# Kernel optimization log

Hardware: AMD Instinct MI355X
Metric: run time of the kernel (lower is better)

## Reference

```python
import jax, jax.numpy as jnp
import numpy as np
from jax import lax

# program token ids
PAD, START, END, SCENE, INTERSECT, FILT, RELATE, QUERY = range(8)
SKIP = (PAD, START, END)


def conv2d(x, w, b, dil=1):
    # 'same' padding for odd kernels (3x3 pad=dil, 1x1 pad=0), NCHW/OIHW
    pad = dil * (w.shape[2] // 2)
    y = lax.conv_general_dilated(x, w, (1, 1), [(pad, pad), (pad, pad)],
                                 rhs_dilation=(dil, dil),
                                 dimension_numbers=('NCHW', 'OIHW', 'NCHW'))
    return y + b[None, :, None, None]


def maxpool2(x):
    return lax.reduce_window(x, -jnp.inf, lax.max, (1, 1, 2, 2), (1, 1, 2, 2), 'VALID')


def exec_program(prog, feat_input, p):
    """Run one (concrete) program over a batch of stem features. prog: tuple of ints,
    executed in reversed order exactly like TbDNet.forward."""
    B, _, H, W = feat_input.shape
    output = feat_input
    saved = None
    for t in reversed(prog):
        if t in SKIP:
            continue
        if t == SCENE:
            saved = output
            output = jnp.ones((B, 1, H, W), feat_input.dtype)
        elif t == INTERSECT:  # AndModule: elementwise min of attentions
            output = jnp.minimum(output, saved)
        elif t == FILT:
            a = feat_input * output  # [B,D,H,W] * [B,1,H,W]
            a = jax.nn.relu(conv2d(a, p['att_w1'], p['att_b1']))
            a = jax.nn.relu(conv2d(a, p['att_w2'], p['att_b2']))
            output = jax.nn.sigmoid(conv2d(a, p['att_w3'], p['att_b3']))
        elif t == RELATE:  # RelateModule: dilated conv stack (1,2,4,8,1) -> conv1x1 sigmoid
            a = feat_input * output
            for w, b, d in ((p['rel_w1'], p['rel_b1'], 1), (p['rel_w2'], p['rel_b2'], 2),
                            (p['rel_w3'], p['rel_b3'], 4), (p['rel_w4'], p['rel_b4'], 8),
                            (p['rel_w5'], p['rel_b5'], 1)):
                a = jax.nn.relu(conv2d(a, w, b, d))
            output = jax.nn.sigmoid(conv2d(a, p['rel_w6'], p['rel_b6']))
        elif t == QUERY:
            a = feat_input * output
            a = jax.nn.relu(conv2d(a, p['qry_w1'], p['qry_b1']))
            output = jax.nn.relu(conv2d(a, p['qry_w2'], p['qry_b2']))
    return output


def tbd_forward(feats, programs_np, p):
    B = feats.shape[0]
    stem = jax.nn.relu(conv2d(feats, p['stem_w1'], p['stem_b1']))
    stem = jax.nn.relu(conv2d(stem, p['stem_w2'], p['stem_b2']))  # [B,D,H,W]
    D, H, W = stem.shape[1], stem.shape[2], stem.shape[3]
    # group samples by identical program so dispatch runs batched, not per-sample
    groups = {}
    for n in range(B):
        groups.setdefault(tuple(int(v) for v in programs_np[n]), []).append(n)
    mod_out = jnp.zeros((B, D, H, W), feats.dtype)
    for prog, idxs in groups.items():
        idx = jnp.array(idxs)
        mod_out = mod_out.at[idx].set(exec_program(prog, stem[idx], p))
    # classifier: conv1x1 -> relu -> maxpool2 -> flatten -> fc -> relu -> fc
    x = jax.nn.relu(conv2d(mod_out, p['cls_w'], p['cls_b']))
    x = maxpool2(x)                        # [B,1024,7,7]
    x = x.reshape(B, -1)                   # [B,50176]
    x = jax.nn.relu(x @ p['fc1_w'].T + p['fc1_b'])
    return x @ p['fc2_w'].T + p['fc2_b']   # [B,28]


def setup_inputs() -> dict:
    key = jax.random.key(0)
    ks = iter(jax.random.split(key, 64))
    def rn(shape, s=0.05):
        return jax.random.normal(next(ks), shape, dtype=jnp.float32) * s
    B, Cin, H, W, D, P, L, A = 64, 1024, 14, 14, 128, 1024, 1024, 28
    feats = jax.random.normal(next(ks), (B, Cin, H, W), dtype=jnp.float32)
    # stored programs; execution order is reversed(stored)
    progA = [START, QUERY, FILT, RELATE, FILT, SCENE, END, PAD]            # scene->filter->relate->filter->query
    progB = [START, QUERY, INTERSECT, FILT, SCENE, FILT, SCENE, END]       # two filter branches -> intersect -> query
    programs = jnp.array([progA] * (B // 2) + [progB] * (B // 2), dtype=jnp.int32)
    inp = {'feats': feats, 'programs': programs,
           'stem_w1': rn((D, Cin, 3, 3), 0.02), 'stem_b1': rn((D,)),
           'stem_w2': rn((D, D, 3, 3)), 'stem_b2': rn((D,)),
           'att_w1': rn((D, D, 3, 3)), 'att_b1': rn((D,)),
           'att_w2': rn((D, D, 3, 3)), 'att_b2': rn((D,)),
           'att_w3': rn((1, D, 1, 1)), 'att_b3': rn((1,)),
           'rel_w1': rn((D, D, 3, 3)), 'rel_b1': rn((D,)),
           'rel_w2': rn((D, D, 3, 3)), 'rel_b2': rn((D,)),
           'rel_w3': rn((D, D, 3, 3)), 'rel_b3': rn((D,)),
           'rel_w4': rn((D, D, 3, 3)), 'rel_b4': rn((D,)),
           'rel_w5': rn((D, D, 3, 3)), 'rel_b5': rn((D,)),
           'rel_w6': rn((1, D, 1, 1)), 'rel_b6': rn((1,)),
           'qry_w1': rn((D, D, 3, 3)), 'qry_b1': rn((D,)),
           'qry_w2': rn((D, D, 3, 3)), 'qry_b2': rn((D,)),
           'cls_w': rn((P, D, 1, 1)), 'cls_b': rn((P,)),
           'fc1_w': rn((L, P * (H // 2) * (W // 2)), 0.01), 'fc1_b': rn((L,)),
           'fc2_w': rn((A, L)), 'fc2_b': rn((A,))}
    return inp


PARAM_NAMES = ['stem_w1', 'stem_b1', 'stem_w2', 'stem_b2',
               'att_w1', 'att_b1', 'att_w2', 'att_b2', 'att_w3', 'att_b3',
               'rel_w1', 'rel_b1', 'rel_w2', 'rel_b2', 'rel_w3', 'rel_b3',
               'rel_w4', 'rel_b4', 'rel_w5', 'rel_b5', 'rel_w6', 'rel_b6',
               'qry_w1', 'qry_b1', 'qry_w2', 'qry_b2',
               'cls_w', 'cls_b', 'fc1_w', 'fc1_b', 'fc2_w', 'fc2_b']


def reference(feats, programs, stem_w1, stem_b1, stem_w2, stem_b2,
              att_w1, att_b1, att_w2, att_b2, att_w3, att_b3,
              rel_w1, rel_b1, rel_w2, rel_b2, rel_w3, rel_b3,
              rel_w4, rel_b4, rel_w5, rel_b5, rel_w6, rel_b6,
              qry_w1, qry_b1, qry_w2, qry_b2,
              cls_w, cls_b, fc1_w, fc1_b, fc2_w, fc2_b):
    vals = [stem_w1, stem_b1, stem_w2, stem_b2,
            att_w1, att_b1, att_w2, att_b2, att_w3, att_b3,
            rel_w1, rel_b1, rel_w2, rel_b2, rel_w3, rel_b3,
            rel_w4, rel_b4, rel_w5, rel_b5, rel_w6, rel_b6,
            qry_w1, qry_b1, qry_w2, qry_b2,
            cls_w, cls_b, fc1_w, fc1_b, fc2_w, fc2_b]
    p = dict(zip(PARAM_NAMES, vals))
    return tbd_forward(feats, np.asarray(programs), p)
```

## Files before the change

### kernel.cpp

```cpp
#include <hip/hip_runtime.h>
#include <math.h>


typedef __attribute__((ext_vector_type(8)))  short   short8;
typedef __attribute__((ext_vector_type(8)))  __bf16  bf16x8;
typedef __attribute__((ext_vector_type(4)))  float   f32x4;

#define NROUNDS 11
#define NKS 98
#define S1KS 16

#define B_WSTEM1 0UL
#define B_WSTEM2 2359296UL
#define B_WMOD   2654208UL
#define B_WCLS   5308416UL
#define B_STEM   5570560UL
#define B_XA     8781824UL
#define B_XB     11993088UL
#define B_FEAT   15204352UL
#define B_ATTN   18415616UL
#define B_SAVED  18465792UL
#define B_SCHED  18515968UL
#define B_ACTB   18520064UL
#define B_FC1T   24942592UL
#define B_P1X1   25204736UL
#define B_S1P    67108864UL
#define B_FC1P   134217728UL

__device__ __forceinline__ unsigned short f2bf(float f) {
    __bf16 h = (__bf16)f;
    union { __bf16 h; unsigned short u; } c; c.h = h; return c.u;
}
__device__ __forceinline__ float bf2f(unsigned short u) {
    return __uint_as_float(((unsigned int)u) << 16);
}
__device__ __forceinline__ unsigned int pkbf(float a, float b) {
    return (unsigned int)f2bf(a) | ((unsigned int)f2bf(b) << 16);
}
__device__ __forceinline__ f32x4 mfma16(bf16x8 a, bf16x8 b, f32x4 c) {
    return __builtin_amdgcn_mfma_f32_16x16x32_bf16(a, b, c, 0, 0, 0);
}

struct PrepArgs { const float* src[12]; const int* prog; char* ws; };

__global__ __launch_bounds__(256) void k_prep(PrepArgs a)
{
    char* ws = a.ws;
    const int bx = blockIdx.x;
    if (bx < 768) {
        const int y = bx >> 6;
        const float* __restrict__ src = a.src[y];
        int gid = (bx & 63) * 256 + threadIdx.x;
        int gsz = 64 * 256;
        if (y == 11) {
            unsigned short* dst = (unsigned short*)(ws + B_WCLS);
            for (int i = gid; i < 131072; i += gsz) dst[i] = f2bf(src[i]);
        } else {
            const int IC = (y == 0) ? 1024 : 128;
            const int lg = (y == 0) ? 10 : 7;
            unsigned short* dst = (unsigned short*)(ws + ((y == 0) ? B_WSTEM1
                                        : (y == 1) ? B_WSTEM2
                                        : B_WMOD + (size_t)(y - 2) * 294912));
            const int total = 9 << (lg + 7);
            for (int i = gid; i < total; i += gsz) {
                int ic = i & (IC - 1);
                int oc = (i >> lg) & 127;
                int t  = i >> (lg + 7);
                dst[i] = f2bf(src[((size_t)oc * IC + ic) * 9 + t]);
            }
        }
        return;
    }
    int gid = (bx - 768) * 256 + threadIdx.x;
    int gsz = 256 * 256;
    float* attn  = (float*)(ws + B_ATTN);
    float* saved = (float*)(ws + B_SAVED);
    float* p1    = (float*)(ws + B_P1X1);
    for (int i = gid; i < 64 * 196; i += gsz) { attn[i] = 1.0f; saved[i] = 1.0f; }
    for (int i = gid; i < 8 * 64 * 196; i += gsz) p1[i] = 0.0f;
    unsigned int* fz = (unsigned int*)(ws + B_FEAT);
    for (int i = gid; i < 64 * 25088 / 2; i += gsz) fz[i] = 0u;
    if (gid < 64) {
        int n = gid;
        const int* prog = a.prog;
        int ent[NROUNDS];
        for (int r = 0; r < NROUNDS; ++r) ent[r] = 0;
        int rc = 0, nslot = 0;
        int pscene = 0, pinter = 0, pmat = 0, pmw = 0;
#define PREBITS ((pscene<<17)|(pinter<<18)|(pmat<<19)|(pmw<<22))
#define CLRPRE  (pscene = pinter = pmat = pmw = 0)
#define EMIT(v) do { if (rc < NROUNDS) ent[rc++] = (v); } while (0)
        for (int j = 7; j >= 0; --j) {
            int t = prog[n * 8 + j];
            switch (t) {
                case 3: pscene = 1; break;
                case 4: pinter = 1; break;
                case 5: {
                    int e1 = 3 | (0<<4) | (1<<8) | (1<<12) | (2<<13) | (0<<15) | PREBITS;
                    CLRPRE; EMIT(e1);
                    EMIT(3 | (1<<4) | (1<<8) | (0<<12) | (0<<13) | (1<<15)
                           | (1<<23) | (0<<24) | (nslot<<25));
                    pmat = nslot + 1; pmw = 0; nslot++;
                    break;
                }
                case 6: {
                    int e1 = 3 | (2<<4) | (1<<8) | (1<<12) | (2<<13) | (0<<15) | PREBITS;
                    CLRPRE; EMIT(e1);
                    EMIT(3 | (3<<4) | (2<<8) | (0<<12) | (0<<13) | (1<<15));
                    EMIT(3 | (4<<4) | (4<<8) | (0<<12) | (1<<13) | (0<<15));
                    EMIT(3 | (5<<4) | (8<<8) | (0<<12) | (0<<13) | (1<<15));
                    EMIT(3 | (6<<4) | (1<<8) | (0<<12) | (1<<13) | (0<<15)
                           | (1<<23) | (1<<24) | (nslot<<25));
                    pmat = nslot + 1; pmw = 1; nslot++;
                    break;
                }
                case 7: {
                    int e1 = 3 | (7<<4) | (1<<8) | (1<<12) | (2<<13) | (0<<15) | PREBITS;
                    CLRPRE; EMIT(e1);
                    EMIT(3 | (8<<4) | (1<<8) | (0<<12) | (0<<13) | (2<<15));
                    break;
                }
                default: break;
            }
        }
#undef EMIT
#undef PREBITS
#undef CLRPRE
        int* sched = (int*)(ws + B_SCHED);
        for (int r = 0; r < NROUNDS; ++r) sched[n * NROUNDS + r] = ent[r];
    }
}

__global__ __launch_bounds__(512) void k_stem1p(const float* __restrict__ feats,
                                                const unsigned short* __restrict__ wrep,
                                                char* ws)
{
    __shared__ unsigned short s_img[197 * 72];
    const int bx = blockIdx.x;
    const int n = bx >> 4, ks = bx & 15;
    const int tid = threadIdx.x, lane = tid & 63;
    const int w = tid >> 6, wm = w & 1, wn = w >> 1;
    const int l15 = lane & 15, lq = lane >> 4;

    if (tid < 36) ((unsigned int*)(s_img + 196 * 72))[tid] = 0u;

    int pglob[4], pbyt[4], pyv[4], pxv[4];
#pragma unroll
    for (int j = 0; j < 4; ++j) {
        int p  = (wn + 4 * j) * 16 + l15;
        pglob[j] = p;
        int py = p / 14;
        pyv[j] = (p < 196) ? py : 10000;
        pxv[j] = p - py * 14;
        pbyt[j] = p * 144 + lq * 16;
    }
    const int zaddr = 196 * 144 + lq * 16;
    const int nJ = (wn == 0) ? 4 : 3;

    f32x4 acc[4][4];
#pragma unroll
    for (int m = 0; m < 4; ++m)
#pragma unroll
        for (int j = 0; j < 4; ++j) acc[m][j] = (f32x4){0.f, 0.f, 0.f, 0.f};

    const int icg = tid & 15;
    const int qq0 = tid >> 4;
    const int icb = ks * 64;

    const float* sf = feats + ((size_t)n * 1024 + icb) * 196;
    for (int qq = qq0; qq < 49; qq += 32) {
        const float* p0 = sf + icg * 4 * 196 + qq * 4;
        float4 r0 = *(const float4*)(p0);
        float4 r1 = *(const float4*)(p0 + 196);
        float4 r2 = *(const float4*)(p0 + 392);
        float4 r3 = *(const float4*)(p0 + 588);
#pragma unroll
        for (int e = 0; e < 4; ++e) {
            uint2 v;
            v.x = pkbf(((const float*)&r0)[e], ((const float*)&r1)[e]);
            v.y = pkbf(((const float*)&r2)[e], ((const float*)&r3)[e]);
            *(uint2*)(s_img + (qq * 4 + e) * 72 + icg * 4) = v;
        }
    }
    __syncthreads();

#pragma unroll
    for (int t = 0; t < 9; ++t) {
        const int dy = t / 3 - 1, dx = t % 3 - 1;
        int baddr[4];
#pragma unroll
        for (int j = 0; j < 4; ++j) {
            int yy = pyv[j] + dy, xx = pxv[j] + dx;
            bool ok = ((unsigned)yy < 14u) && ((unsigned)xx < 14u);
            baddr[j] = ok ? (pbyt[j] + (dy * 14 + dx) * 144) : zaddr;
        }
#pragma unroll
        for (int kc = 0; kc < 2; ++kc) {
            const unsigned short* wt = wrep +
                ((size_t)(t * 128 + wm * 64 + l15) * 1024 + icb + kc * 32 + lq * 8);
            bf16x8 am[4];
#pragma unroll
            for (int m = 0; m < 4; ++m)
                am[m] = *(const bf16x8*)(wt + (size_t)m * 16 * 1024);
#pragma unroll
            for (int j = 0; j < 4; ++j) {
                if (j < nJ) {
                    bf16x8 b = *(const bf16x8*)((const char*)s_img + baddr[j] + kc * 64);
#pragma unroll
                    for (int m = 0; m < 4; ++m)
                        acc[m][j] = mfma16(am[m], b, acc[m][j]);
                }
            }
        }
    }

    unsigned short* part = (unsigned short*)(ws + B_S1P);
#pragma unroll
    for (int m = 0; m < 4; ++m) {
        const int oc = wm * 64 + m * 16 + lq * 4;
#pragma unroll
        for (int j = 0; j < 4; ++j) {
            if (j < nJ) {
                int p = pglob[j];
                if (p < 196) {
                    uint2 pk;
                    pk.x = pkbf(acc[m][j][0], acc[m][j][1]);
                    pk.y = pkbf(acc[m][j][2], acc[m][j][3]);
                    *(uint2*)(part + (((size_t)ks * 64 + n) * 196 + p) * 128 + oc) = pk;
                }
            }
        }
    }
}

__global__ __launch_bounds__(256) void k_stem1r(const char* __restrict__ ws_c,
                                                const float* __restrict__ bias,
                                                unsigned short* __restrict__ xa)
{
    int i = blockIdx.x * 256 + threadIdx.x;
    const unsigned short* part = (const unsigned short*)(ws_c + B_S1P);
    int oc8 = (i & 15) * 8;
    int np  = i >> 4;
    float s[8] = {};
#pragma unroll
    for (int ks = 0; ks < S1KS; ++ks) {
        short8 v = *(const short8*)(part + (((size_t)ks * 64) * 196 + np) * 128 + oc8);
#pragma unroll
        for (int e = 0; e < 8; ++e) s[e] += bf2f((unsigned short)v[e]);
    }
    short8 o;
#pragma unroll
    for (int e = 0; e < 8; ++e)
        o[e] = (short)f2bf(fmaxf(s[e] + bias[oc8 + e], 0.f));
    *(short8*)(xa + (size_t)np * 128 + oc8) = o;
}

__device__ void conv_core32(const unsigned short* __restrict__ srcB,
                            const float* __restrict__ s_gate,
                            const unsigned short* __restrict__ wrep,
                            const float* __restrict__ bias,
                            unsigned short* __restrict__ dst,
                            int dil, int oct, int pxh,
                            unsigned short* s_img,
                            int post, const float* __restrict__ pwv,
                            float* __restrict__ pdst)
{
    const int tid  = threadIdx.x, lane = tid & 63;
    const int w    = tid >> 6, wm = w & 1, wn = w >> 1;
    const int l15  = lane & 15, lq = lane >> 4;

    if (tid < 68) ((unsigned int*)s_img)[196 * 68 + tid] = 0u;

    int pglob[4], pbyt[4], pyv[4], pxv[4];
#pragma unroll
    for (int j = 0; j < 4; ++j) {
        int nt = wn + 2 * j;
        int p  = (pxh * 7 + nt) * 16 + l15;
        pglob[j] = p;
        int py = p / 14;
        pyv[j] = (p < 196) ? py : 10000;
        pxv[j] = p - py * 14;
        pbyt[j] = p * 272 + lq * 16;
    }
    const int zaddr = 196 * 272 + lq * 16;
    const int nNT = (wn == 0) ? 4 : 3;

    f32x4 acc[4];
#pragma unroll
    for (int j = 0; j < 4; ++j) acc[j] = (f32x4){0.f, 0.f, 0.f, 0.f};

    if (s_gate) {
        for (int i = tid; i < 196 * 16; i += 256) {
            int p = i >> 4, c8 = (i & 15) * 8;
            short8 v = *(const short8*)(srcB + p * 128 + c8);
            float g = s_gate[p];
            uint2 o0, o1;
            o0.x = pkbf(bf2f((unsigned short)v[0]) * g, bf2f((unsigned short)v[1]) * g);
            o0.y = pkbf(bf2f((unsigned short)v[2]) * g, bf2f((unsigned short)v[3]) * g);
            o1.x = pkbf(bf2f((unsigned short)v[4]) * g, bf2f((unsigned short)v[5]) * g);
            o1.y = pkbf(bf2f((unsigned short)v[6]) * g, bf2f((unsigned short)v[7]) * g);
            *(uint2*)(s_img + p * 136 + c8)     = o0;
            *(uint2*)(s_img + p * 136 + c8 + 4) = o1;
        }
    } else {
        for (int i = tid; i < 196 * 16; i += 256) {
            int p = i >> 4, c8 = (i & 15) * 8;
            *(short8*)(s_img + p * 136 + c8) = *(const short8*)(srcB + p * 128 + c8);
        }
    }
    __syncthreads();

    const unsigned short* wlane = wrep + (size_t)(oct * 32 + wm * 16 + l15) * 128 + lq * 8;
#pragma unroll
    for (int t = 0; t < 9; ++t) {
        const int dy = (t / 3 - 1) * dil, dx = (t % 3 - 1) * dil;
        int baddr[4];
#pragma unroll
        for (int j = 0; j < 4; ++j) {
            int yy = pyv[j] + dy, xx = pxv[j] + dx;
            bool ok = ((unsigned)yy < 14u) && ((unsigned)xx < 14u);
            baddr[j] = ok ? (pbyt[j] + (dy * 14 + dx) * 272) : zaddr;
        }
        const unsigned short* wt = wlane + (size_t)(t * 128) * 128;
#pragma unroll
        for (int kc = 0; kc < 4; ++kc) {
            bf16x8 a0 = *(const bf16x8*)(wt + kc * 32);
#pragma unroll
            for (int j = 0; j < 4; ++j) {
                if (j < nNT) {
                    bf16x8 b = *(const bf16x8*)((const char*)s_img + baddr[j] + kc * 64);
                    acc[j] = mfma16(a0, b, acc[j]);
                }
            }
        }
    }

    const int oc = oct * 32 + wm * 16 + lq * 4;
    const float4 b4 = *(const float4*)(bias + oc);
    float4 wv4;
    if (post) wv4 = *(const float4*)(pwv + oc);
#pragma unroll
    for (int j = 0; j < 4; ++j) {
        if (j < nNT) {
            int p = pglob[j];
            if (p < 196) {
                float v0 = fmaxf(acc[j][0] + b4.x, 0.f);
                float v1 = fmaxf(acc[j][1] + b4.y, 0.f);
                float v2 = fmaxf(acc[j][2] + b4.z, 0.f);
                float v3 = fmaxf(acc[j][3] + b4.w, 0.f);
                uint2 pk;
                pk.x = pkbf(v0, v1);
                pk.y = pkbf(v2, v3);
                *(uint2*)(dst + p * 128 + oc) = pk;
                if (post) {
                    float s = v0 * wv4.x + v1 * wv4.y + v2 * wv4.z + v3 * wv4.w;
                    atomicAdd(pdst + p, s);
                }
            }
        }
    }
}

__global__ __launch_bounds__(256) void k_conv_stem2(const unsigned short* __restrict__ srcBall,
                                                    const unsigned short* __restrict__ wrep,
                                                    const float* __restrict__ bias,
                                                    unsigned short* __restrict__ dstall)
{
    __shared__ unsigned short s_img[197 * 136];
    const int n = blockIdx.x >> 3, oct = (blockIdx.x >> 1) & 3, pxh = blockIdx.x & 1;
    conv_core32(srcBall + (size_t)n * 25088, nullptr, wrep, bias,
                dstall + (size_t)n * 25088, 1, oct, pxh, s_img, 0, nullptr, nullptr);
}

struct RArgs {
    char* ws;
    const float* mbias[9];
    const float* w1x1[2];
    const float* b1x1[2];
};

__global__ __launch_bounds__(256) void k_round(RArgs a, int r)
{
    __shared__ unsigned short s_img[197 * 136];
    __shared__ float s_gate[196];
    const int bx = blockIdx.x;
    const int n = bx >> 3, oct = (bx >> 1) & 3, pxh = bx & 1;
    char* ws = a.ws;
    const int* sched = (const int*)(ws + B_SCHED);
    const int e = sched[n * NROUNDS + r];
    if ((e & 15) == 0) return;
    const int tid = threadIdx.x;
    const int wset = (e >> 4) & 15, dil = (e >> 8) & 15, gatef = (e >> 12) & 1;
    const int srcid = (e >> 13) & 3, dstid = (e >> 15) & 3;
    const int fscene = (e >> 17) & 1, finter = (e >> 18) & 1;
    const int mslot = (e >> 19) & 7, mw = (e >> 22) & 1;
    const int post = (e >> 23) & 1, pw = (e >> 24) & 1, pslot = (e >> 25) & 7;

    float* attn  = (float*)(ws + B_ATTN)  + n * 196;
    float* saved = (float*)(ws + B_SAVED) + n * 196;
    float* p1    = (float*)(ws + B_P1X1);

    if (gatef) {
        if (tid < 196) {
            float cur = attn[tid];
            if (mslot) {
                float pv = p1[(size_t)(mslot - 1) * 12544 + n * 196 + tid];
                cur = 1.0f / (1.0f + __expf(-(pv + a.b1x1[mw][0])));
            }
            if (fscene) { saved[tid] = cur; cur = 1.0f; }
            if (finter) { cur = fminf(cur, saved[tid]); }
            if (mslot | fscene | finter) attn[tid] = cur;
            s_gate[tid] = cur;
        }
        __syncthreads();
    }

    const unsigned short* src = (const unsigned short*)(ws +
            (srcid == 2 ? B_STEM : srcid == 1 ? B_XB : B_XA)) + (size_t)n * 25088;
    unsigned short* dst = (unsigned short*)(ws +
            (dstid == 2 ? B_FEAT : dstid == 1 ? B_XB : B_XA)) + (size_t)n * 25088;
    const unsigned short* wrep = (const unsigned short*)(ws + B_WMOD) + (size_t)wset * 9 * 128 * 128;

    conv_core32(src, gatef ? s_gate : nullptr, wrep, a.mbias[wset], dst,
                dil, oct, pxh, s_img,
                post, post ? a.w1x1[pw] : nullptr,
                post ? (p1 + (size_t)pslot * 12544 + n * 196) : nullptr);
}

__global__ __launch_bounds__(256) void k_cls_pool(const unsigned short* __restrict__ featall,
                                                  const unsigned short* __restrict__ clsw,
                                                  const float* __restrict__ clsb,
                                                  unsigned short* __restrict__ actB)
{
    __shared__ char smem[197 * 272 + 64 * 200 * 4];
    unsigned short* s_img = (unsigned short*)smem;
    float* s_pool = (float*)(smem + 197 * 272);
    const int n = blockIdx.x >> 4, pt = blockIdx.x & 15;
    const int tid = threadIdx.x, lane = tid & 63, w = tid >> 6;
    const int l15 = lane & 15, lq = lane >> 4;
    const unsigned short* feat = featall + (size_t)n * 25088;

    if (tid < 68) ((unsigned int*)s_img)[196 * 68 + tid] = 0u;
    for (int i = tid; i < 196 * 16; i += 256) {
        int p = i >> 4, c8 = (i & 15) * 8;
        *(short8*)(s_img + p * 136 + c8) = *(const short8*)(feat + p * 128 + c8);
    }
    f32x4 acc[14];
#pragma unroll
    for (int j = 0; j < 14; ++j) acc[j] = (f32x4){0.f, 0.f, 0.f, 0.f};
    __syncthreads();

    const unsigned short* wl = clsw + (size_t)(pt * 64 + w * 16 + l15) * 128 + lq * 8;
#pragma unroll
    for (int kc = 0; kc < 4; ++kc) {
        bf16x8 a0 = *(const bf16x8*)(wl + kc * 32);
#pragma unroll
        for (int j = 0; j < 14; ++j) {
            int p = j * 16 + l15;
            int ba = (p < 196) ? (p * 272 + lq * 16 + kc * 64) : (196 * 272 + lq * 16);
            bf16x8 b = *(const bf16x8*)((const char*)s_img + ba);
            acc[j] = mfma16(a0, b, acc[j]);
        }
    }
    const int oc = pt * 64 + w * 16 + lq * 4;
    const float4 b4 = *(const float4*)(clsb + oc);
    const int pl = w * 16 + lq * 4;
#pragma unroll
    for (int j = 0; j < 14; ++j) {
        int p = j * 16 + l15;
        if (p < 196) {
            s_pool[(pl + 0) * 200 + p] = fmaxf(acc[j][0] + b4.x, 0.f);
            s_pool[(pl + 1) * 200 + p] = fmaxf(acc[j][1] + b4.y, 0.f);
            s_pool[(pl + 2) * 200 + p] = fmaxf(acc[j][2] + b4.z, 0.f);
            s_pool[(pl + 3) * 200 + p] = fmaxf(acc[j][3] + b4.w, 0.f);
        }
    }
    __syncthreads();
    for (int i = tid; i < 64 * 49; i += 256) {
        int plx = i / 49, q = i - plx * 49;
        int py = q / 7, qx = q - py * 7;
        const float* rp = s_pool + plx * 200 + py * 28 + qx * 2;
        float m = fmaxf(fmaxf(rp[0], rp[1]), fmaxf(rp[14], rp[15]));
        int k = (pt * 64 + plx) * 49 + q;
        int kb = k >> 6, lq2 = (k >> 4) & 3, hi = (k >> 3) & 1, e = k & 7;
        actB[((((size_t)kb * 4 + lq2) * 2 + hi) * 64 + n) * 8 + e] = f2bf(m);
    }
}

__global__ __launch_bounds__(256) void k_fc1p(const unsigned short* __restrict__ actB,
                                              const float* __restrict__ w,
                                              float* __restrict__ part)
{
    __shared__ unsigned short s_w[64 * 264];
    const int jt = blockIdx.x & 15, ks = blockIdx.x >> 4;
    const int tid = threadIdx.x, lane = tid & 63, wv = tid >> 6;
    const int l15 = lane & 15, lq = lane >> 4;
    const int k0 = ks * 512;

    f32x4 acc[4];
#pragma unroll
    for (int t = 0; t < 4; ++t) acc[t] = (f32x4){0.f, 0.f, 0.f, 0.f};

    float4 pf[16];

#define FC1_LOAD(ss_) do {                                                        \
    _Pragma("unroll")                                                             \
    for (int pass = 0; pass < 16; ++pass) {                                       \
        const int row_ = pass * 4 + wv;                                           \
        pf[pass] = *(const float4*)(w + (size_t)(jt * 64 + row_) * 50176 + k0     \
                                      + (ss_) * 256 + lane * 4);                  \
    } } while (0)

    FC1_LOAD(0);

    for (int ss = 0; ss < 2; ++ss) {
        __syncthreads();
#pragma unroll
        for (int pass = 0; pass < 16; ++pass) {
            const int row = pass * 4 + wv;
            uint2 v;
            v.x = pkbf(pf[pass].x, pf[pass].y);
            v.y = pkbf(pf[pass].z, pf[pass].w);
            *(uint2*)(s_w + row * 264 + lane * 4) = v;
        }
        __syncthreads();
        if (ss < 1) FC1_LOAD(1);

        const unsigned short* arow = s_w + (wv * 16 + l15) * 264;
#pragma unroll
        for (int kk = 0; kk < 8; ++kk) {
            bf16x8 a = *(const bf16x8*)(arow + kk * 32 + lq * 8);
            const int kglob = k0 + ss * 256 + kk * 32 + lq * 8;
            const int kb = kglob >> 6, lq2 = (kglob >> 4) & 3, hi = (kglob >> 3) & 1;
            const unsigned short* bp = actB +
                ((((size_t)kb * 4 + lq2) * 2 + hi) * 64 + l15) * 8;
#pragma unroll
            for (int t = 0; t < 4; ++t) {
                bf16x8 b = *(const bf16x8*)(bp + t * 128);
                acc[t] = mfma16(a, b, acc[t]);
            }
        }
    }
#undef FC1_LOAD

    float* pbase = part + ((size_t)ks * 1024 + jt * 64 + wv * 16 + lq * 4) * 64 + l15;
#pragma unroll
    for (int t = 0; t < 4; ++t)
#pragma unroll
        for (int r = 0; r < 4; ++r)
            pbase[(size_t)r * 64 + t * 16] = acc[t][r];
}

__global__ __launch_bounds__(256) void k_fc1r(const float* __restrict__ part,
                                              const float* __restrict__ b,
                                              float* __restrict__ fc1T)
{
    int i = blockIdx.x * 256 + threadIdx.x;
    if (i >= 65536) return;
    float s = 0.0f;
    for (int ks = 0; ks < NKS; ++ks) s += part[(size_t)ks * 65536 + i];
    int j = i >> 6;
    fc1T[i] = fmaxf(s + b[j], 0.0f);
}

__global__ __launch_bounds__(256) void k_fc2(const float* __restrict__ fc1T,
                                             const float* __restrict__ w,
                                             const float* __restrict__ b,
                                             float* __restrict__ out)
{
    __shared__ float red[256];
    const int a_ = blockIdx.x;
    const int tid = threadIdx.x, lane = tid & 63, q = tid >> 6;
    float acc = 0.0f;
    const float* wr = w + (size_t)a_ * 1024;
    for (int k = q * 256; k < q * 256 + 256; ++k)
        acc = fmaf(fc1T[k * 64 + lane], wr[k], acc);
    red[tid] = acc;
    __syncthreads();
    if (q == 0) {
        float s = red[tid] + red[tid + 64] + red[tid + 128] + red[tid + 192] + b[a_];
        out[lane * 28 + a_] = s;
    }
}

extern "C" void kernel_launch(void* const* d_in, const int* in_sizes, int n_in,
                              void* d_out, int out_size, void* d_ws, size_t ws_size,
                              hipStream_t stream)
{
    const float* feats = (const float*)d_in[0];
    const int*   prog  = (const int*)d_in[1];
    char* ws  = (char*)d_ws;
    float* out = (float*)d_out;

    PrepArgs pa;
    pa.src[0]  = (const float*)d_in[2];
    pa.src[1]  = (const float*)d_in[4];
    pa.src[2]  = (const float*)d_in[6];
    pa.src[3]  = (const float*)d_in[8];
    pa.src[4]  = (const float*)d_in[12];
    pa.src[5]  = (const float*)d_in[14];
    pa.src[6]  = (const float*)d_in[16];
    pa.src[7]  = (const float*)d_in[18];
    pa.src[8]  = (const float*)d_in[20];
    pa.src[9]  = (const float*)d_in[24];
    pa.src[10] = (const float*)d_in[26];
    pa.src[11] = (const float*)d_in[28];
    pa.prog = prog;
    pa.ws = ws;
    k_prep<<<1024, 256, 0, stream>>>(pa);

    k_stem1p<<<1024, 512, 0, stream>>>(feats, (const unsigned short*)(ws + B_WSTEM1), ws);
    k_stem1r<<<784, 256, 0, stream>>>(ws, (const float*)d_in[3],
                                      (unsigned short*)(ws + B_XA));

    k_conv_stem2<<<512, 256, 0, stream>>>((const unsigned short*)(ws + B_XA),
                                          (const unsigned short*)(ws + B_WSTEM2),
                                          (const float*)d_in[5],
                                          (unsigned short*)(ws + B_STEM));

    RArgs ga;
    ga.ws = ws;
    ga.mbias[0] = (const float*)d_in[7];
    ga.mbias[1] = (const float*)d_in[9];
    ga.mbias[2] = (const float*)d_in[13];
    ga.mbias[3] = (const float*)d_in[15];
    ga.mbias[4] = (const float*)d_in[17];
    ga.mbias[5] = (const float*)d_in[19];
    ga.mbias[6] = (const float*)d_in[21];
    ga.mbias[7] = (const float*)d_in[25];
    ga.mbias[8] = (const float*)d_in[27];
    ga.w1x1[0]  = (const float*)d_in[10];
    ga.w1x1[1]  = (const float*)d_in[22];
    ga.b1x1[0]  = (const float*)d_in[11];
    ga.b1x1[1]  = (const float*)d_in[23];

    for (int r = 0; r < NROUNDS; ++r)
        k_round<<<512, 256, 0, stream>>>(ga, r);

    k_cls_pool<<<1024, 256, 0, stream>>>((const unsigned short*)(ws + B_FEAT),
                                         (const unsigned short*)(ws + B_WCLS),
                                         (const float*)d_in[29],
                                         (unsigned short*)(ws + B_ACTB));
    k_fc1p<<<1568, 256, 0, stream>>>((const unsigned short*)(ws + B_ACTB),
                                     (const float*)d_in[30], (float*)(ws + B_FC1P));
    k_fc1r<<<256, 256, 0, stream>>>((const float*)(ws + B_FC1P), (const float*)d_in[31],
                                    (float*)(ws + B_FC1T));
    k_fc2<<<28, 256, 0, stream>>>((const float*)(ws + B_FC1T), (const float*)d_in[32],
                                  (const float*)d_in[33], out);
}
```

Measured before the change: 514.7 us.

## Fuse paired 3x3 convs of Filter/Query modules into one round via shared-memory intermediate

Adds a fused op (op 5) that runs the first conv of the attention and query modules over all 128 output channels into shared memory, then runs the second conv from that buffer. This cuts the schedule from 11 to 8 rounds and avoids a global round-trip for the intermediate activation. Each block now handles a whole image with 512 threads, with 256 blocks instead of 512. In exchange the first conv is recomputed redundantly in each of the 4 output-channel blocks, and fewer blocks run per launch.

```diff
diff --git a/kernel.cpp b/kernel.cpp
--- a/kernel.cpp
+++ b/kernel.cpp
@@ -6,7 +6,7 @@
 typedef __attribute__((ext_vector_type(8)))  __bf16  bf16x8;
 typedef __attribute__((ext_vector_type(4)))  float   f32x4;
 
-#define NROUNDS 11
+#define NROUNDS 8
 #define NKS 98
 #define S1KS 16
 
@@ -96,28 +96,26 @@
                 case 3: pscene = 1; break;
                 case 4: pinter = 1; break;
                 case 5: {
-                    int e1 = 3 | (0<<4) | (1<<8) | (1<<12) | (2<<13) | (0<<15) | PREBITS;
+                    int e1 = 5 | (0<<4) | (1<<8) | (1<<12) | (0<<15) | PREBITS
+                               | (1<<23) | (0<<24) | (nslot<<25);
                     CLRPRE; EMIT(e1);
-                    EMIT(3 | (1<<4) | (1<<8) | (0<<12) | (0<<13) | (1<<15)
-                           | (1<<23) | (0<<24) | (nslot<<25));
                     pmat = nslot + 1; pmw = 0; nslot++;
                     break;
                 }
                 case 6: {
                     int e1 = 3 | (2<<4) | (1<<8) | (1<<12) | (2<<13) | (0<<15) | PREBITS;
                     CLRPRE; EMIT(e1);
-                    EMIT(3 | (3<<4) | (2<<8) | (0<<12) | (0<<13) | (1<<15));
-                    EMIT(3 | (4<<4) | (4<<8) | (0<<12) | (1<<13) | (0<<15));
-                    EMIT(3 | (5<<4) | (8<<8) | (0<<12) | (0<<13) | (1<<15));
-                    EMIT(3 | (6<<4) | (1<<8) | (0<<12) | (1<<13) | (0<<15)
+                    EMIT(3 | (3<<4) | (2<<8) | (0<<13) | (1<<15));
+                    EMIT(3 | (4<<4) | (4<<8) | (1<<13) | (0<<15));
+                    EMIT(3 | (5<<4) | (8<<8) | (0<<13) | (1<<15));
+                    EMIT(3 | (6<<4) | (1<<8) | (1<<13) | (0<<15)
                            | (1<<23) | (1<<24) | (nslot<<25));
                     pmat = nslot + 1; pmw = 1; nslot++;
                     break;
                 }
                 case 7: {
-                    int e1 = 3 | (7<<4) | (1<<8) | (1<<12) | (2<<13) | (0<<15) | PREBITS;
+                    int e1 = 5 | (7<<4) | (8<<8) | (1<<12) | (2<<15) | PREBITS;
                     CLRPRE; EMIT(e1);
-                    EMIT(3 | (8<<4) | (1<<8) | (0<<12) | (0<<13) | (2<<15));
                     break;
                 }
                 default: break;
@@ -256,14 +254,11 @@
 }
 
 __device__ void conv_core32(const unsigned short* __restrict__ srcB,
-                            const float* __restrict__ s_gate,
                             const unsigned short* __restrict__ wrep,
                             const float* __restrict__ bias,
                             unsigned short* __restrict__ dst,
-                            int dil, int oct, int pxh,
-                            unsigned short* s_img,
-                            int post, const float* __restrict__ pwv,
-                            float* __restrict__ pdst)
+                            int oct, int pxh,
+                            unsigned short* s_img)
 {
     const int tid  = threadIdx.x, lane = tid & 63;
     const int w    = tid >> 6, wm = w & 1, wn = w >> 1;
@@ -289,10 +284,210 @@
 #pragma unroll
     for (int j = 0; j < 4; ++j) acc[j] = (f32x4){0.f, 0.f, 0.f, 0.f};
 
-    if (s_gate) {
-        for (int i = tid; i < 196 * 16; i += 256) {
+    for (int i = tid; i < 196 * 16; i += 256) {
+        int p = i >> 4, c8 = (i & 15) * 8;
+        *(short8*)(s_img + p * 136 + c8) = *(const short8*)(srcB + p * 128 + c8);
+    }
+    __syncthreads();
+
+    const unsigned short* wlane = wrep + (size_t)(oct * 32 + wm * 16 + l15) * 128 + lq * 8;
+#pragma unroll
+    for (int t = 0; t < 9; ++t) {
+        const int dy = t / 3 - 1, dx = t % 3 - 1;
+        int baddr[4];
+#pragma unroll
+        for (int j = 0; j < 4; ++j) {
+            int yy = pyv[j] + dy, xx = pxv[j] + dx;
+            bool ok = ((unsigned)yy < 14u) && ((unsigned)xx < 14u);
+            baddr[j] = ok ? (pbyt[j] + (dy * 14 + dx) * 272) : zaddr;
+        }
+        const unsigned short* wt = wlane + (size_t)(t * 128) * 128;
+#pragma unroll
+        for (int kc = 0; kc < 4; ++kc) {
+            bf16x8 a0 = *(const bf16x8*)(wt + kc * 32);
+#pragma unroll
+            for (int j = 0; j < 4; ++j) {
+                if (j < nNT) {
+                    bf16x8 b = *(const bf16x8*)((const char*)s_img + baddr[j] + kc * 64);
+                    acc[j] = mfma16(a0, b, acc[j]);
+                }
+            }
+        }
+    }
+
+    const int oc = oct * 32 + wm * 16 + lq * 4;
+    const float4 b4 = *(const float4*)(bias + oc);
+#pragma unroll
+    for (int j = 0; j < 4; ++j) {
+        if (j < nNT) {
+            int p = pglob[j];
+            if (p < 196) {
+                uint2 pk;
+                pk.x = pkbf(fmaxf(acc[j][0] + b4.x, 0.f), fmaxf(acc[j][1] + b4.y, 0.f));
+                pk.y = pkbf(fmaxf(acc[j][2] + b4.z, 0.f), fmaxf(acc[j][3] + b4.w, 0.f));
+                *(uint2*)(dst + p * 128 + oc) = pk;
+            }
+        }
+    }
+}
+
+__global__ __launch_bounds__(256) void k_conv_stem2(const unsigned short* __restrict__ srcBall,
+                                                    const unsigned short* __restrict__ wrep,
+                                                    const float* __restrict__ bias,
+                                                    unsigned short* __restrict__ dstall)
+{
+    __shared__ unsigned short s_img[197 * 136];
+    const int n = blockIdx.x >> 3, oct = (blockIdx.x >> 1) & 3, pxh = blockIdx.x & 1;
+    conv_core32(srcBall + (size_t)n * 25088, wrep, bias,
+                dstall + (size_t)n * 25088, oct, pxh, s_img);
+}
+
+struct RArgs {
+    char* ws;
+    const float* mbias[9];
+    const float* w1x1[2];
+    const float* b1x1[2];
+};
+
+__global__ __launch_bounds__(512) void k_round(RArgs a, int r)
+{
+    __shared__ unsigned short s_img[197 * 136];
+    __shared__ unsigned short s_tmp[197 * 136];
+    __shared__ float s_gate[196];
+    const int bx = blockIdx.x;
+    const int n = bx >> 2, oct = bx & 3;
+    char* ws = a.ws;
+    const int* sched = (const int*)(ws + B_SCHED);
+    const int e = sched[n * NROUNDS + r];
+    const int op = e & 15;
+    if (op == 0) return;
+    const int tid = threadIdx.x, lane = tid & 63;
+    const int w = tid >> 6, wm = w & 1, wn = w >> 1;
+    const int l15 = lane & 15, lq = lane >> 4;
+    const int wset1 = (e >> 4) & 15, f8 = (e >> 8) & 15, gatef = (e >> 12) & 1;
+    const int srcid = (e >> 13) & 3, dstid = (e >> 15) & 3;
+    const int fscene = (e >> 17) & 1, finter = (e >> 18) & 1;
+    const int mslot = (e >> 19) & 7, mw = (e >> 22) & 1;
+    const int post = (e >> 23) & 1, pw = (e >> 24) & 1, pslot = (e >> 25) & 7;
+
+    float* attn  = (float*)(ws + B_ATTN)  + n * 196;
+    float* saved = (float*)(ws + B_SAVED) + n * 196;
+    float* p1    = (float*)(ws + B_P1X1);
+
+    if (tid < 68) ((unsigned int*)s_img)[196 * 68 + tid] = 0u;
+    else if (tid < 136) ((unsigned int*)s_tmp)[196 * 68 + (tid - 68)] = 0u;
+
+    if (gatef && tid < 196) {
+        float cur = attn[tid];
+        if (mslot) {
+            float pv = p1[(size_t)(mslot - 1) * 12544 + n * 196 + tid];
+            cur = 1.0f / (1.0f + __expf(-(pv + a.b1x1[mw][0])));
+        }
+        if (fscene) { saved[tid] = cur; cur = 1.0f; }
+        if (finter) { cur = fminf(cur, saved[tid]); }
+        if (mslot | fscene | finter) attn[tid] = cur;
+        s_gate[tid] = cur;
+    }
+    __syncthreads();
+
+    const int zaddr = 196 * 272 + lq * 16;
+    const unsigned short* wmod = (const unsigned short*)(ws + B_WMOD);
+
+    if (op == 3) {
+        const unsigned short* src = (const unsigned short*)(ws +
+                (srcid == 2 ? B_STEM : srcid == 1 ? B_XB : B_XA)) + (size_t)n * 25088;
+        if (gatef) {
+            for (int i = tid; i < 196 * 16; i += 512) {
+                int p = i >> 4, c8 = (i & 15) * 8;
+                short8 v = *(const short8*)(src + p * 128 + c8);
+                float g = s_gate[p];
+                uint2 o0, o1;
+                o0.x = pkbf(bf2f((unsigned short)v[0]) * g, bf2f((unsigned short)v[1]) * g);
+                o0.y = pkbf(bf2f((unsigned short)v[2]) * g, bf2f((unsigned short)v[3]) * g);
+                o1.x = pkbf(bf2f((unsigned short)v[4]) * g, bf2f((unsigned short)v[5]) * g);
+                o1.y = pkbf(bf2f((unsigned short)v[6]) * g, bf2f((unsigned short)v[7]) * g);
+                *(uint2*)(s_img + p * 136 + c8)     = o0;
+                *(uint2*)(s_img + p * 136 + c8 + 4) = o1;
+            }
+        } else {
+            for (int i = tid; i < 196 * 16; i += 512) {
+                int p = i >> 4, c8 = (i & 15) * 8;
+                *(short8*)(s_img + p * 136 + c8) = *(const short8*)(src + p * 128 + c8);
+            }
+        }
+        __syncthreads();
+
+        int pglob[4], pbyt[4], pyv[4], pxv[4];
+#pragma unroll
+        for (int j = 0; j < 4; ++j) {
+            int p = (wn + 4 * j) * 16 + l15;
+            pglob[j] = p;
+            int py = p / 14;
+            pyv[j] = (p < 196) ? py : 10000;
+            pxv[j] = p - py * 14;
+            pbyt[j] = p * 272 + lq * 16;
+        }
+        const int nJ = (wn == 0) ? 4 : 3;
+        f32x4 acc[4];
+#pragma unroll
+        for (int j = 0; j < 4; ++j) acc[j] = (f32x4){0.f, 0.f, 0.f, 0.f};
+
+        const int dil = f8;
+        const unsigned short* wlane = wmod + (size_t)wset1 * 147456 / 2 * 0;
+        wlane = wmod + (size_t)wset1 * 9 * 128 * 128
+                     + (size_t)(oct * 32 + wm * 16 + l15) * 128 + lq * 8;
+#pragma unroll
+        for (int t = 0; t < 9; ++t) {
+            const int dy = (t / 3 - 1) * dil, dx = (t % 3 - 1) * dil;
+            int ba[4];
+#pragma unroll
+            for (int j = 0; j < 4; ++j) {
+                int yy = pyv[j] + dy, xx = pxv[j] + dx;
+                bool ok = ((unsigned)yy < 14u) && ((unsigned)xx < 14u);
+                ba[j] = ok ? (pbyt[j] + (dy * 14 + dx) * 272) : zaddr;
+            }
+            const unsigned short* wt = wlane + (size_t)(t * 128) * 128;
+#pragma unroll
+            for (int kc = 0; kc < 4; ++kc) {
+                bf16x8 a0 = *(const bf16x8*)(wt + kc * 32);
+#pragma unroll
+                for (int j = 0; j < 4; ++j) {
+                    if (j < nJ) {
+                        bf16x8 b = *(const bf16x8*)((const char*)s_img + ba[j] + kc * 64);
+                        acc[j] = mfma16(a0, b, acc[j]);
+                    }
+                }
+            }
+        }
+
+        unsigned short* dst = (unsigned short*)(ws +
+                (dstid == 2 ? B_FEAT : dstid == 1 ? B_XB : B_XA)) + (size_t)n * 25088;
+        const int oc = oct * 32 + wm * 16 + lq * 4;
+        const float4 b4 = *(const float4*)(a.mbias[wset1] + oc);
+        float4 wv4;
+        if (post) wv4 = *(const float4*)(a.w1x1[pw] + oc);
+        float* pdst = p1 + (size_t)pslot * 12544 + n * 196;
+#pragma unroll
+        for (int j = 0; j < 4; ++j) {
+            if (j < nJ) {
+                int p = pglob[j];
+                if (p < 196) {
+                    float v0 = fmaxf(acc[j][0] + b4.x, 0.f);
+                    float v1 = fmaxf(acc[j][1] + b4.y, 0.f);
+                    float v2 = fmaxf(acc[j][2] + b4.z, 0.f);
+                    float v3 = fmaxf(acc[j][3] + b4.w, 0.f);
+                    uint2 pk; pk.x = pkbf(v0, v1); pk.y = pkbf(v2, v3);
+                    *(uint2*)(dst + p * 128 + oc) = pk;
+                    if (post)
+                        atomicAdd(pdst + p, v0 * wv4.x + v1 * wv4.y + v2 * wv4.z + v3 * wv4.w);
+                }
+            }
+        }
+    } else {
+        const unsigned short* stem = (const unsigned short*)(ws + B_STEM) + (size_t)n * 25088;
+        for (int i = tid; i < 196 * 16; i += 512) {
             int p = i >> 4, c8 = (i & 15) * 8;
-            short8 v = *(const short8*)(srcB + p * 128 + c8);
+            short8 v = *(const short8*)(stem + p * 128 + c8);
             float g = s_gate[p];
             uint2 o0, o1;
             o0.x = pkbf(bf2f((unsigned short)v[0]) * g, bf2f((unsigned short)v[1]) * g);
@@ -302,129 +497,125 @@
             *(uint2*)(s_img + p * 136 + c8)     = o0;
             *(uint2*)(s_img + p * 136 + c8 + 4) = o1;
         }
-    } else {
-        for (int i = tid; i < 196 * 16; i += 256) {
-            int p = i >> 4, c8 = (i & 15) * 8;
-            *(short8*)(s_img + p * 136 + c8) = *(const short8*)(srcB + p * 128 + c8);
-        }
-    }
-    __syncthreads();
-
-    const unsigned short* wlane = wrep + (size_t)(oct * 32 + wm * 16 + l15) * 128 + lq * 8;
-#pragma unroll
-    for (int t = 0; t < 9; ++t) {
-        const int dy = (t / 3 - 1) * dil, dx = (t % 3 - 1) * dil;
-        int baddr[4];
+        __syncthreads();
+
+        const unsigned short* w1 = wmod + (size_t)wset1 * 9 * 128 * 128;
+        int pg2[13], pb2[13], pyv2[13], pxv2[13];
+#pragma unroll
+        for (int j2 = 0; j2 < 13; ++j2) {
+            int p = j2 * 16 + l15;
+            pg2[j2] = p;
+            int py = p / 14;
+            pyv2[j2] = (p < 196) ? py : 10000;
+            pxv2[j2] = p - py * 14;
+            pb2[j2] = p * 272 + lq * 16;
+        }
+        f32x4 acc1[13];
+#pragma unroll
+        for (int j2 = 0; j2 < 13; ++j2) acc1[j2] = (f32x4){0.f, 0.f, 0.f, 0.f};
+#pragma unroll
+        for (int t = 0; t < 9; ++t) {
+            const int dy = t / 3 - 1, dx = t % 3 - 1;
+            int ba[13];
+#pragma unroll
+            for (int j2 = 0; j2 < 13; ++j2) {
+                int yy = pyv2[j2] + dy, xx = pxv2[j2] + dx;
+                bool ok = ((unsigned)yy < 14u) && ((unsigned)xx < 14u);
+                ba[j2] = ok ? (pb2[j2] + (dy * 14 + dx) * 272) : zaddr;
+            }
+#pragma unroll
+            for (int kc = 0; kc < 4; ++kc) {
+                bf16x8 av = *(const bf16x8*)(w1 +
+                    (size_t)(t * 128 + w * 16 + l15) * 128 + kc * 32 + lq * 8);
+#pragma unroll
+                for (int j2 = 0; j2 < 13; ++j2) {
+                    bf16x8 b = *(const bf16x8*)((const char*)s_img + ba[j2] + kc * 64);
+                    acc1[j2] = mfma16(av, b, acc1[j2]);
+                }
+            }
+        }
+        {
+            const int oc1 = w * 16 + lq * 4;
+            const float4 b14 = *(const float4*)(a.mbias[wset1] + oc1);
+#pragma unroll
+            for (int j2 = 0; j2 < 13; ++j2) {
+                int p = pg2[j2];
+                if (p < 196) {
+                    uint2 pk;
+                    pk.x = pkbf(fmaxf(acc1[j2][0] + b14.x, 0.f),
+                                fmaxf(acc1[j2][1] + b14.y, 0.f));
+                    pk.y = pkbf(fmaxf(acc1[j2][2] + b14.z, 0.f),
+                                fmaxf(acc1[j2][3] + b14.w, 0.f));
+                    *(uint2*)(s_tmp + p * 136 + oc1) = pk;
+                }
+            }
+        }
+        __syncthreads();
+
+        const unsigned short* w2base = wmod + (size_t)f8 * 9 * 128 * 128
+                     + (size_t)(oct * 32 + wm * 16 + l15) * 128 + lq * 8;
+        int pglob[4], pbyt[4], pyv[4], pxv[4];
 #pragma unroll
         for (int j = 0; j < 4; ++j) {
-            int yy = pyv[j] + dy, xx = pxv[j] + dx;
-            bool ok = ((unsigned)yy < 14u) && ((unsigned)xx < 14u);
-            baddr[j] = ok ? (pbyt[j] + (dy * 14 + dx) * 272) : zaddr;
-        }
-        const unsigned short* wt = wlane + (size_t)(t * 128) * 128;
-#pragma unroll
-        for (int kc = 0; kc < 4; ++kc) {
-            bf16x8 a0 = *(const bf16x8*)(wt + kc * 32);
+            int p = (wn + 4 * j) * 16 + l15;
+            pglob[j] = p;
+            int py = p / 14;
+            pyv[j] = (p < 196) ? py : 10000;
+            pxv[j] = p - py * 14;
+            pbyt[j] = p * 272 + lq * 16;
+        }
+        const int nJ = (wn == 0) ? 4 : 3;
+        f32x4 acc[4];
+#pragma unroll
+        for (int j = 0; j < 4; ++j) acc[j] = (f32x4){0.f, 0.f, 0.f, 0.f};
+#pragma unroll
+        for (int t = 0; t < 9; ++t) {
+            const int dy = t / 3 - 1, dx = t % 3 - 1;
+            int ba[4];
 #pragma unroll
             for (int j = 0; j < 4; ++j) {
-                if (j < nNT) {
-                    bf16x8 b = *(const bf16x8*)((const char*)s_img + baddr[j] + kc * 64);
-                    acc[j] = mfma16(a0, b, acc[j]);
-                }
-            }
-        }
-    }
-
-    const int oc = oct * 32 + wm * 16 + lq * 4;
-    const float4 b4 = *(const float4*)(bias + oc);
-    float4 wv4;
-    if (post) wv4 = *(const float4*)(pwv + oc);
-#pragma unroll
-    for (int j = 0; j < 4; ++j) {
-        if (j < nNT) {
-            int p = pglob[j];
-            if (p < 196) {
-                float v0 = fmaxf(acc[j][0] + b4.x, 0.f);
-                float v1 = fmaxf(acc[j][1] + b4.y, 0.f);
-                float v2 = fmaxf(acc[j][2] + b4.z, 0.f);
-                float v3 = fmaxf(acc[j][3] + b4.w, 0.f);
-                uint2 pk;
-                pk.x = pkbf(v0, v1);
-                pk.y = pkbf(v2, v3);
-                *(uint2*)(dst + p * 128 + oc) = pk;
-                if (post) {
-                    float s = v0 * wv4.x + v1 * wv4.y + v2 * wv4.z + v3 * wv4.w;
-                    atomicAdd(pdst + p, s);
-                }
-            }
-        }
-    }
-}
-
-__global__ __launch_bounds__(256) void k_conv_stem2(const unsigned short* __restrict__ srcBall,
-                                                    const unsigned short* __restrict__ wrep,
-                                                    const float* __restrict__ bias,
-                                                    unsigned short* __restrict__ dstall)
-{
-    __shared__ unsigned short s_img[197 * 136];
-    const int n = blockIdx.x >> 3, oct = (blockIdx.x >> 1) & 3, pxh = blockIdx.x & 1;
-    conv_core32(srcBall + (size_t)n * 25088, nullptr, wrep, bias,
-                dstall + (size_t)n * 25088, 1, oct, pxh, s_img, 0, nullptr, nullptr);
-}
-
-struct RArgs {
-    char* ws;
-    const float* mbias[9];
-    const float* w1x1[2];
-    const float* b1x1[2];
-};
-
-__global__ __launch_bounds__(256) void k_round(RArgs a, int r)
-{
-    __shared__ unsigned short s_img[197 * 136];
-    __shared__ float s_gate[196];
-    const int bx = blockIdx.x;
-    const int n = bx >> 3, oct = (bx >> 1) & 3, pxh = bx & 1;
-    char* ws = a.ws;
-    const int* sched = (const int*)(ws + B_SCHED);
-    const int e = sched[n * NROUNDS + r];
-    if ((e & 15) == 0) return;
-    const int tid = threadIdx.x;
-    const int wset = (e >> 4) & 15, dil = (e >> 8) & 15, gatef = (e >> 12) & 1;
-    const int srcid = (e >> 13) & 3, dstid = (e >> 15) & 3;
-    const int fscene = (e >> 17) & 1, finter = (e >> 18) & 1;
-    const int mslot = (e >> 19) & 7, mw = (e >> 22) & 1;
-    const int post = (e >> 23) & 1, pw = (e >> 24) & 1, pslot = (e >> 25) & 7;
-
-    float* attn  = (float*)(ws + B_ATTN)  + n * 196;
-    float* saved = (float*)(ws + B_SAVED) + n * 196;
-    float* p1    = (float*)(ws + B_P1X1);
-
-    if (gatef) {
-        if (tid < 196) {
-            float cur = attn[tid];
-            if (mslot) {
-                float pv = p1[(size_t)(mslot - 1) * 12544 + n * 196 + tid];
-                cur = 1.0f / (1.0f + __expf(-(pv + a.b1x1[mw][0])));
-            }
-            if (fscene) { saved[tid] = cur; cur = 1.0f; }
-            if (finter) { cur = fminf(cur, saved[tid]); }
-            if (mslot | fscene | finter) attn[tid] = cur;
-            s_gate[tid] = cur;
-        }
-        __syncthreads();
-    }
-
-    const unsigned short* src = (const unsigned short*)(ws +
-            (srcid == 2 ? B_STEM : srcid == 1 ? B_XB : B_XA)) + (size_t)n * 25088;
-    unsigned short* dst = (unsigned short*)(ws +
-            (dstid == 2 ? B_FEAT : dstid == 1 ? B_XB : B_XA)) + (size_t)n * 25088;
-    const unsigned short* wrep = (const unsigned short*)(ws + B_WMOD) + (size_t)wset * 9 * 128 * 128;
-
-    conv_core32(src, gatef ? s_gate : nullptr, wrep, a.mbias[wset], dst,
-                dil, oct, pxh, s_img,
-                post, post ? a.w1x1[pw] : nullptr,
-                post ? (p1 + (size_t)pslot * 12544 + n * 196) : nullptr);
+                int yy = pyv[j] + dy, xx = pxv[j] + dx;
+                bool ok = ((unsigned)yy < 14u) && ((unsigned)xx < 14u);
+                ba[j] = ok ? (pbyt[j] + (dy * 14 + dx) * 272) : zaddr;
+            }
+            const unsigned short* wt = w2base + (size_t)(t * 128) * 128;
+#pragma unroll
+            for (int kc = 0; kc < 4; ++kc) {
+                bf16x8 a0 = *(const bf16x8*)(wt + kc * 32);
+#pragma unroll
+                for (int j = 0; j < 4; ++j) {
+                    if (j < nJ) {
+                        bf16x8 b = *(const bf16x8*)((const char*)s_tmp + ba[j] + kc * 64);
+                        acc[j] = mfma16(a0, b, acc[j]);
+                    }
+                }
+            }
+        }
+        const int oc = oct * 32 + wm * 16 + lq * 4;
+        const float4 b24 = *(const float4*)(a.mbias[f8] + oc);
+        unsigned short* feat = (unsigned short*)(ws + B_FEAT) + (size_t)n * 25088;
+        float4 wv4;
+        if (post) wv4 = *(const float4*)(a.w1x1[pw] + oc);
+        float* pdst = p1 + (size_t)pslot * 12544 + n * 196;
+#pragma unroll
+        for (int j = 0; j < 4; ++j) {
+            if (j < nJ) {
+                int p = pglob[j];
+                if (p < 196) {
+                    float v0 = fmaxf(acc[j][0] + b24.x, 0.f);
+                    float v1 = fmaxf(acc[j][1] + b24.y, 0.f);
+                    float v2 = fmaxf(acc[j][2] + b24.z, 0.f);
+                    float v3 = fmaxf(acc[j][3] + b24.w, 0.f);
+                    if (dstid == 2) {
+                        uint2 pk; pk.x = pkbf(v0, v1); pk.y = pkbf(v2, v3);
+                        *(uint2*)(feat + p * 128 + oc) = pk;
+                    }
+                    if (post)
+                        atomicAdd(pdst + p, v0 * wv4.x + v1 * wv4.y + v2 * wv4.z + v3 * wv4.w);
+                }
+            }
+        }
+    }
 }
 
 __global__ __launch_bounds__(256) void k_cls_pool(const unsigned short* __restrict__ featall,
@@ -635,7 +826,7 @@
     ga.b1x1[1]  = (const float*)d_in[23];
 
     for (int r = 0; r < NROUNDS; ++r)
-        k_round<<<512, 256, 0, stream>>>(ga, r);
+        k_round<<<256, 512, 0, stream>>>(ga, r);
 
     k_cls_pool<<<1024, 256, 0, stream>>>((const unsigned short*)(ws + B_FEAT),
                                          (const unsigned short*)(ws + B_WCLS),
```

New measurement: 511.8 us. About the same (-0.6%).
